# Kernel tuning notes

Measured on AMD Instinct MI355X. Metric: run time of the kernel, lower is better.

## Reference

```python
import jax, jax.numpy as jnp
import numpy as np
from math import ceil

N = 20000   # nodes
E = 320000  # edges
D = 128     # num_features == num_hidden
K = ceil(N * 0.1)  # 2000 PMA seeds


def _gcn(x, W, b, src, dst):
    # PyG GCNConv: add self-loops, symmetric deg^-1/2 normalization, sum-aggregate, bias
    n = x.shape[0]
    sl = jnp.arange(n)
    s = jnp.concatenate([src, sl])
    d = jnp.concatenate([dst, sl])
    deg = jax.ops.segment_sum(jnp.ones((s.shape[0],), x.dtype), d, num_segments=n)
    dinv = jax.lax.rsqrt(jnp.maximum(deg, 1e-12))
    norm = dinv[s] * dinv[d]
    h = x @ W
    return jax.ops.segment_sum(h[s] * norm[:, None], d, num_segments=n) + b


def _ln(x, g, b):
    m = jnp.mean(x, -1, keepdims=True)
    v = jnp.var(x, -1, keepdims=True)
    return (x - m) * jax.lax.rsqrt(v + 1e-5) * g + b


def setup_inputs() -> dict:
    key = jax.random.key(0)
    ks = jax.random.split(key, 32)
    w = lambda i, shape: jax.random.normal(ks[i], shape, jnp.float32) * 0.05
    z = lambda shape: jnp.zeros(shape, jnp.float32)
    o = lambda shape: jnp.ones(shape, jnp.float32)
    return {
        "x": jax.random.normal(ks[0], (N, D), jnp.float32),
        "edge_index": jax.random.randint(ks[1], (2, E), 0, N),
        "batch": jnp.zeros((N,), jnp.int32),
        "W1": w(2, (D, D)), "b1": z((D,)),
        "W2": w(3, (D, D)), "b2": z((D,)),
        "S": w(4, (1, K, D)),
        "Wq": w(5, (D, D)), "bq": z((D,)),
        "Wk": w(6, (D, D)), "bk": z((D,)),
        "Wv": w(7, (D, D)), "bv": z((D,)),
        "Wo": w(8, (D, D)), "bo": z((D,)),
        "g0": o((D,)), "be0": z((D,)),
        "g1": o((D,)), "be1": z((D,)),
        "Wl": w(9, (D, D)), "bl": z((D,)),
        "W3": w(10, (D, D)), "b3": z((D,)),
        "W4": w(11, (D, D)), "b4": z((D,)),
        "W5": w(12, (D, D)), "b5": z((D,)),
    }


def reference(x, edge_index, batch, W1, b1, W2, b2, S, Wq, bq, Wk, bk, Wv, bv,
              Wo, bo, g0, be0, g1, be1, Wl, bl, W3, b3, W4, b4, W5, b5):
    src, dst = edge_index[0], edge_index[1]
    h = jax.nn.relu(_gcn(x, W1, b1, src, dst))
    h = jax.nn.relu(_gcn(h, W2, b2, src, dst))
    # B=1 dense batch: mask all-true -> additive attention mask is 0
    Q = S @ Wq + bq                        # [1,K,D]
    Kd = _gcn(h, Wk, bk, src, dst)[None]   # [1,N,D]  (mab_conv='GCN')
    Vd = _gcn(h, Wv, bv, src, dst)[None]   # [1,N,D]
    score = jnp.einsum('bkd,bnd->bkn', Q, Kd) / jnp.sqrt(jnp.float32(D))
    A = jax.nn.softmax(score, axis=1)      # cluster=True: softmax over seed dim
    out = Q + jnp.einsum('bkn,bnd->bkd', A, Vd)
    out = _ln(out, g0, be0)
    out = out + jax.nn.relu(out @ Wo + bo)
    out = _ln(out, g1, be1)
    xl = out @ Wl + bl                     # [1,K,D]
    x_out = jnp.einsum('bkn,bkd->bnd', A, xl)[0]  # attn^T @ x -> [N,D], mask all-true
    h = jax.nn.relu(_gcn(x_out, W3, b3, src, dst))
    h = jax.nn.relu(_gcn(h, W4, b4, src, dst))
    return _gcn(h, W5, b5, src, dst)       # [N,D]
```

## Files before the change

kernel.cpp:

```cpp
#include <hip/hip_runtime.h>

#define NN 20000
#define EE 320000
#define KK 2000
#define KP 2048
#define SCALE 0.08838834764831845f
#define ZSPLIT 16
#define ACHUNKS 625
#define ZCH 4

typedef const float* cfp;
typedef __attribute__((ext_vector_type(8))) short sh8;
typedef __attribute__((ext_vector_type(4))) float f32x4;

static __device__ __forceinline__ float4 ld4(const float* p){ return *reinterpret_cast<const float4*>(p); }
static __device__ __forceinline__ void st4(float* p, float4 v){ *reinterpret_cast<float4*>(p) = v; }

static __device__ __forceinline__ unsigned short f2bf(float f){
    unsigned int u = __float_as_uint(f);
    u = (u + 0x7FFFu + ((u >> 16) & 1u)) >> 16;
    return (unsigned short)u;
}
static __device__ __forceinline__ float bf2f(unsigned short h){
    return __uint_as_float(((unsigned int)h) << 16);
}
static __device__ __forceinline__ sh8 lds8(const unsigned short* p){ return *reinterpret_cast<const sh8*>(p); }

static __device__ __forceinline__ void stage16(const unsigned short* g, unsigned short* l){
    __builtin_amdgcn_global_load_lds(
        (const __attribute__((address_space(1))) unsigned int*)g,
        (__attribute__((address_space(3))) unsigned int*)l, 16, 0, 0);
}

__global__ __launch_bounds__(256) void k_count(const int* dst, int* deg){
    int i = blockIdx.x*256 + threadIdx.x;
    if (i < EE) atomicAdd(&deg[dst[i]], 1);
}

__global__ __launch_bounds__(256) void k_dinv(const int* deg, float* dinv){
    int n = blockIdx.x*256 + threadIdx.x;
    if (n < NN) dinv[n] = rsqrtf((float)deg[n] + 1.0f);
}

__global__ __launch_bounds__(1024) void k_scan(const int* cnt, int* rows){
    __shared__ int part[1024];
    int t = threadIdx.x;
    int base = t*20;
    int s = 0;
    for (int i = 0; i < 20; ++i){ int idx = base+i; if (idx < NN) s += cnt[idx]; }
    part[t] = s; __syncthreads();
    for (int off = 1; off < 1024; off <<= 1){
        int v = (t >= off) ? part[t-off] : 0;
        __syncthreads();
        part[t] += v;
        __syncthreads();
    }
    int run = part[t] - s;
    for (int i = 0; i < 20; ++i){
        int idx = base+i;
        if (idx < NN){ rows[idx] = run; run += cnt[idx]; }
    }
    if (t == 0) rows[NN] = EE;
}

__global__ __launch_bounds__(256) void k_fill(const int* src, const int* dst, const int* rows,
                                              int* cursor, int* col){
    int i = blockIdx.x*256 + threadIdx.x;
    if (i < EE){
        int d = dst[i];
        int pos = rows[d] + atomicAdd(&cursor[d], 1);
        col[pos] = src[i];
    }
}

__global__ __launch_bounds__(256) void conv_wT(cfp w0, cfp w1, cfp w2, cfp w3, cfp w4, cfp w5, cfp w6,
                                               unsigned short* wts){
    const float* in;
    switch (blockIdx.z){
        case 0: in = w0; break; case 1: in = w1; break; case 2: in = w2; break;
        case 3: in = w3; break; case 4: in = w4; break; case 5: in = w5; break;
        default: in = w6; break;
    }
    unsigned short* out = wts + (size_t)blockIdx.z*16384;
    __shared__ float t[64][65];
    int r0 = blockIdx.x*64, c0 = blockIdx.y*64;
    int tid = threadIdx.x;
    for (int i = tid; i < 64*16; i += 256){
        int r = i >> 4, c4 = (i & 15) * 4;
        float4 v = ld4(in + (size_t)(r0+r)*128 + c0 + c4);
        t[r][c4+0]=v.x; t[r][c4+1]=v.y; t[r][c4+2]=v.z; t[r][c4+3]=v.w;
    }
    __syncthreads();
    for (int i = tid; i < 64*16; i += 256){
        int c = i >> 4, r4 = (i & 15) * 4;
        ushort4 o;
        o.x = f2bf(t[r4+0][c]); o.y = f2bf(t[r4+1][c]);
        o.z = f2bf(t[r4+2][c]); o.w = f2bf(t[r4+3][c]);
        *reinterpret_cast<ushort4*>(out + (size_t)(c0+c)*128 + r0 + r4) = o;
    }
}

__global__ __launch_bounds__(512) void gemm128(const float* __restrict__ A, const float* __restrict__ Wm,
                                               float* __restrict__ C, int M,
                                               const float* bias, const float* resid, int relu){
    __shared__ __align__(16) float Ws[128*132];
    __shared__ float As[64*129];
    int tid = threadIdx.x;
    int r0 = blockIdx.x*64;
    for (int i = tid; i < 128*32; i += 512){
        int r = i >> 5, c4 = (i & 31) * 4;
        float4 v = ld4(Wm + r*128 + c4);
        st4(&Ws[r*132 + c4], v);
    }
    for (int i = tid; i < 64*32; i += 512){
        int r = i >> 5, c4 = (i & 31) * 4;
// ... 96 lines not shown
    if (wid >= NN) return;
    int f = lane*2;
    ushort2 u = *reinterpret_cast<const ushort2*>(y + (size_t)wid*128 + f);
    float ax = bf2f(u.x), ay = bf2f(u.y);
    int s = rows[wid], e = rows[wid+1];
    int j = s;
    int e8 = s + ((e - s) & ~7);
    for (; j < e8; j += 8){
        ushort2 v[8];
        #pragma unroll
        for (int q = 0; q < 8; ++q){
            int c = col[j+q];
            v[q] = *reinterpret_cast<const ushort2*>(y + (size_t)c*128 + f);
        }
        #pragma unroll
        for (int q = 0; q < 8; ++q){ ax += bf2f(v[q].x); ay += bf2f(v[q].y); }
    }
    for (; j < e; ++j){
        int c0 = col[j];
        ushort2 v0 = *reinterpret_cast<const ushort2*>(y + (size_t)c0*128 + f);
        ax += bf2f(v0.x); ay += bf2f(v0.y);
    }
    float dn = dinv[wid];
    float ox = ax*dn + bias[f];
    float oy = ay*dn + bias[f+1];
    if (relu){ ox = fmaxf(ox, 0.f); oy = fmaxf(oy, 0.f); }
    if (out_fp32){
        *reinterpret_cast<float2*>((float*)outv + (size_t)wid*128 + f) = make_float2(ox, oy);
    } else {
        ushort2 o; o.x = f2bf(ox); o.y = f2bf(oy);
        *reinterpret_cast<ushort2*>((unsigned short*)outv + (size_t)wid*128 + f) = o;
    }
}

__global__ __launch_bounds__(256) void conv_bf16(const float* __restrict__ in, unsigned short* __restrict__ out, int n4){
    int i = blockIdx.x*256 + threadIdx.x;
    if (i < n4){
        float4 v = ld4(in + (size_t)i*4);
        ushort4 o;
        o.x = f2bf(v.x); o.y = f2bf(v.y); o.z = f2bf(v.z); o.w = f2bf(v.w);
        *reinterpret_cast<ushort4*>(out + (size_t)i*4) = o;
    }
}

__global__ __launch_bounds__(256) void conv_bf16_T(const float* __restrict__ in, unsigned short* __restrict__ out,
                                                   int M, int ldout, const float* __restrict__ rscale){
    __shared__ float t[64][65];
    int r0 = blockIdx.x*64, c0 = blockIdx.y*64;
    int tid = threadIdx.x;
    for (int i = tid; i < 64*16; i += 256){
        int r = i >> 4, c4 = (i & 15) * 4;
        float4 v = (r0 + r < M) ? ld4(in + (size_t)(r0+r)*128 + c0 + c4) : make_float4(0,0,0,0);
        if (rscale && r0 + r < M){
            float sc = rscale[r0 + r];
            v.x *= sc; v.y *= sc; v.z *= sc; v.w *= sc;
        }
        t[r][c4+0]=v.x; t[r][c4+1]=v.y; t[r][c4+2]=v.z; t[r][c4+3]=v.w;
    }
    __syncthreads();
    for (int i = tid; i < 64*16; i += 256){
        int c = i >> 4, r4 = (i & 15) * 4;
        if (r0 + r4 < M){
            ushort4 o;
            o.x = f2bf(t[r4+0][c]); o.y = f2bf(t[r4+1][c]);
            o.z = f2bf(t[r4+2][c]); o.w = f2bf(t[r4+3][c]);
            *reinterpret_cast<ushort4*>(out + (size_t)(c0+c)*ldout + r0 + r4) = o;
        }
    }
}

__global__ __launch_bounds__(256) void k_rcp32(const float* __restrict__ zp, const float* __restrict__ dinv,
                                               float* __restrict__ zinv, float* __restrict__ zdinv){
    int n = blockIdx.x*256 + threadIdx.x;
    if (n < NN){
        float s = 0.f;
        #pragma unroll
        for (int y = 0; y < ZCH; ++y) s += zp[(size_t)y*NN + n];
        float zi = 1.f / s;
        zinv[n] = zi;
        zdinv[n] = zi * dinv[n];
    }
}

__global__ __launch_bounds__(256) void s_gemm_exp(const unsigned short* __restrict__ Kb,
                                                  const unsigned short* __restrict__ Qb2,
                                                  unsigned short* __restrict__ E, float* __restrict__ zpart){
    __shared__ unsigned short Es[4][32*36];
    __shared__ float zsh[2][64];
    int tid = threadIdx.x;
    int wave = tid >> 6, lane = tid & 63;
    int wm = wave >> 1, wn = wave & 1;
    int n_blk = blockIdx.x*64;
    int k_base = blockIdx.y*512;
    int l15 = lane & 15;
    int h = lane >> 4;
    int roff = h * 8;
    int rq = h * 4;
    unsigned short* myEs = Es[wave];
    const unsigned short* ap0 = Kb + (size_t)(n_blk + wm*32 + l15)*128 + roff;
    const unsigned short* ap1 = ap0 + 16*128;
    sh8 a0[4], a1[4];
    #pragma unroll
    for (int r = 0; r < 4; ++r){ a0[r] = lds8(ap0 + r*32); a1[r] = lds8(ap1 + r*32); }
    const unsigned short* qbase = Qb2 + (size_t)(k_base + wn*32 + l15)*128 + roff;
    sh8 q0[4], q1[4];
    #pragma unroll
    for (int r = 0; r < 4; ++r){ q0[r] = lds8(qbase + r*32); q1[r] = lds8(qbase + 16*128 + r*32); }
    float zacc[2][4] = {{0.f,0.f,0.f,0.f},{0.f,0.f,0.f,0.f}};
    for (int kb = 0; kb < 8; ++kb){
        sh8 n0[4], n1[4];
        if (kb < 7){
            const unsigned short* qn = qbase + (size_t)(kb+1)*64*128;
            #pragma unroll
            for (int r = 0; r < 4; ++r){ n0[r] = lds8(qn + r*32); n1[r] = lds8(qn + 16*128 + r*32); }
        } else {
            #pragma unroll
            for (int r = 0; r < 4; ++r){ n0[r] = (sh8)0; n1[r] = (sh8)0; }
        }
        f32x4 acc00 = (f32x4)0.f, acc01 = (f32x4)0.f, acc10 = (f32x4)0.f, acc11 = (f32x4)0.f;
        #pragma unroll
        for (int r = 0; r < 4; ++r){
            acc00 = __builtin_amdgcn_mfma_f32_16x16x32_bf16(a0[r], q0[r], acc00, 0, 0, 0);
            acc01 = __builtin_amdgcn_mfma_f32_16x16x32_bf16(a0[r], q1[r], acc01, 0, 0, 0);
            acc10 = __builtin_amdgcn_mfma_f32_16x16x32_bf16(a1[r], q0[r], acc10, 0, 0, 0);
            acc11 = __builtin_amdgcn_mfma_f32_16x16x32_bf16(a1[r], q1[r], acc11, 0, 0, 0);
        }
        int kcol = k_base + kb*64;
        f32x4 accs[2][2] = {{acc00, acc01},{acc10, acc11}};
        #pragma unroll
        for (int mi = 0; mi < 2; ++mi){
            #pragma unroll
            for (int ni = 0; ni < 2; ++ni){
                f32x4 a = accs[mi][ni];
                bool kv = (kcol + wn*32 + ni*16 + l15) < KK;
                #pragma unroll
                for (int reg = 0; reg < 4; ++reg){
                    float e = kv ? __expf(a[reg]*SCALE) : 0.f;
                    myEs[(mi*16 + rq + reg)*36 + ni*16 + l15] = f2bf(e);
                    zacc[mi][reg] += e;
                }
            }
        }
        #pragma unroll
        for (int it = 0; it < 2; ++it){
            int r = it*16 + (lane >> 2);
            int q4 = (lane & 3) * 8;
            sh8 v = lds8(myEs + r*36 + q4);
            int gr = n_blk + wm*32 + r;
            if (gr < NN)
                *reinterpret_cast<sh8*>(E + (size_t)gr*KP + kcol + wn*32 + q4) = v;
        }
        #pragma unroll
        for (int r = 0; r < 4; ++r){ q0[r] = n0[r]; q1[r] = n1[r]; }
    }
    #pragma unroll
    for (int mi = 0; mi < 2; ++mi){
        #pragma unroll
        for (int reg = 0; reg < 4; ++reg){
            float v = zacc[mi][reg];
            v += __shfl_xor(v, 1);
            v += __shfl_xor(v, 2);
            v += __shfl_xor(v, 4);
            v += __shfl_xor(v, 8);
            zacc[mi][reg] = v;
        }
    }
    if (l15 == 0){
        #pragma unroll
        for (int mi = 0; mi < 2; ++mi)
            #pragma unroll
            for (int reg = 0; reg < 4; ++reg)
                zsh[wn][wm*32 + mi*16 + h*4 + reg] = zacc[mi][reg];
    }
    __syncthreads();
    if (tid < 64){
        int n = n_blk + tid;
        if (n < NN) zpart[(size_t)blockIdx.y*NN + n] = zsh[0][tid] + zsh[1][tid];
    }
}

__global__ __launch_bounds__(256) void attn_gemm(const unsigned short* __restrict__ E,
                                                 const unsigned short* __restrict__ Vt,
                                                 float* __restrict__ part){
    __shared__ unsigned short As[64*36];
    int tid = threadIdx.x;
    int wave = tid >> 6, lane = tid & 63;
    int kk0 = blockIdx.x*64;
    int per = (ACHUNKS + ZSPLIT - 1) / ZSPLIT;
    int c0 = blockIdx.y*per;
    int c1 = min(ACHUNKS, c0 + per);
    int l15 = lane & 15;
    int q8 = (lane >> 4) * 8;
    int d0 = wave*32;
    int n_l = tid & 31;
    int k8 = (tid >> 5) * 8;
    f32x4 acc[4][2];
    #pragma unroll
    for (int g = 0; g < 4; ++g){ acc[g][0] = (f32x4)0.f; acc[g][1] = (f32x4)0.f; }
    const unsigned short* ebase = E + (size_t)n_l*KP + kk0 + k8;
    const unsigned short* vb0p = Vt + (size_t)(d0 + l15)*NN + q8;
    const unsigned short* vb1p = vb0p + (size_t)16*NN;
    sh8 etmp = lds8(ebase + (size_t)c0*32*KP);
    sh8 vb0 = lds8(vb0p + c0*32);
    sh8 vb1 = lds8(vb1p + c0*32);
    for (int ch = c0; ch < c1; ++ch){
        unsigned short tmp[8];
        *reinterpret_cast<sh8*>(tmp) = etmp;
        #pragma unroll
        for (int j = 0; j < 8; ++j) As[(k8 + j)*36 + n_l] = tmp[j];
        __syncthreads();
        sh8 etn = (sh8)0, vbn0 = (sh8)0, vbn1 = (sh8)0;
        if (ch + 1 < c1){
            etn  = lds8(ebase + (size_t)(ch+1)*32*KP);
            vbn0 = lds8(vb0p + (ch+1)*32);
            vbn1 = lds8(vb1p + (ch+1)*32);
        }
        #pragma unroll
        for (int g = 0; g < 4; ++g){
            const unsigned short* ap = &As[(g*16 + l15)*36 + q8];
            union { struct { ushort4 lo, hi; } u; sh8 v; } af;
            af.u.lo = *reinterpret_cast<const ushort4*>(ap);
            af.u.hi = *reinterpret_cast<const ushort4*>(ap + 4);
            acc[g][0] = __builtin_amdgcn_mfma_f32_16x16x32_bf16(af.v, vb0, acc[g][0], 0, 0, 0);
            acc[g][1] = __builtin_amdgcn_mfma_f32_16x16x32_bf16(af.v, vb1, acc[g][1], 0, 0, 0);
        }
        __syncthreads();
        etmp = etn; vb0 = vbn0; vb1 = vbn1;
    }
    float* pbase = part + (size_t)blockIdx.y*KK*128;
    int rq = (lane >> 4) * 4;
    #pragma unroll
    for (int g = 0; g < 4; ++g){
        #pragma unroll
        for (int ni = 0; ni < 2; ++ni){
            int d = d0 + ni*16 + l15;
            #pragma unroll
            for (int reg = 0; reg < 4; ++reg){
                int kk = kk0 + g*16 + rq + reg;
                if (kk < KK) pbase[(size_t)kk*128 + d] = acc[g][ni][reg];
            }
        }
    }
}

__global__ __launch_bounds__(256) void xout_gemm(const unsigned short* __restrict__ E,
                                                 const unsigned short* __restrict__ B,
                                                 const float* __restrict__ zdinv,
                                                 unsigned short* __restrict__ out){
    __shared__ __align__(16) unsigned short ebuf[2][4096];
    int tid = threadIdx.x;
    int wave = tid >> 6, lane = tid & 63;
    int l15 = lane & 15;
    int h = lane >> 4;
    int m_base = blockIdx.x*32;
    int srow0 = wave*4 + h;
    int skb0  = (l15*16) ^ ((srow0 & 15) << 4);
    int srow1 = 16 + srow0;
    int skb1  = (l15*16) ^ ((srow1 & 15) << 4);
    const unsigned short* g0 = E + (size_t)(m_base + srow0)*KP + (skb0 >> 1);
    const unsigned short* g1 = E + (size_t)(m_base + srow1)*KP + (skb1 >> 1);
    unsigned short* l0 = &ebuf[0][wave*512];
    unsigned short* l1 = &ebuf[1][wave*512];
    const unsigned short* bp0 = B + (size_t)(wave*32 + l15)*KP + h*8;
    const unsigned short* bp1 = bp0 + (size_t)16*KP;
    int rswz = l15 << 4;

    f32x4 acc[2][2];
    #pragma unroll
    for (int mi = 0; mi < 2; ++mi)
        #pragma unroll
        for (int ni = 0; ni < 2; ++ni) acc[mi][ni] = (f32x4)0.f;

    stage16(g0, l0);
    stage16(g1, l0 + 2048);
    sh8 b0[4], b1[4];
    #pragma unroll
    for (int s = 0; s < 4; ++s){ b0[s] = lds8(bp0 + s*32); b1[s] = lds8(bp1 + s*32); }
    __syncthreads();

    for (int t = 0; t < 16; ++t){
        if (t < 15){
            const unsigned short* ng0 = g0 + (t+1)*128;
            const unsigned short* ng1 = g1 + (t+1)*128;
            unsigned short* nl = (t & 1) ? l0 : l1;
            stage16(ng0, nl);
            stage16(ng1, nl + 2048);
        }
        sh8 nb0[4], nb1[4];
        if (t < 15){
            #pragma unroll
            for (int s = 0; s < 4; ++s){
                nb0[s] = lds8(bp0 + (t+1)*128 + s*32);
                nb1[s] = lds8(bp1 + (t+1)*128 + s*32);
            }
        } else {
            #pragma unroll
            for (int s = 0; s < 4; ++s){ nb0[s] = (sh8)0; nb1[s] = (sh8)0; }
        }
        const unsigned short* eb = (t & 1) ? ebuf[1] : ebuf[0];
        #pragma unroll
        for (int s = 0; s < 4; ++s){
            int ko = ((h*16 + s*64) ^ rswz) >> 1;
            sh8 a0 = lds8(eb + l15*128 + ko);
            sh8 a1 = lds8(eb + (16 + l15)*128 + ko);
            acc[0][0] = __builtin_amdgcn_mfma_f32_16x16x32_bf16(a0, b0[s], acc[0][0], 0, 0, 0);
            acc[0][1] = __builtin_amdgcn_mfma_f32_16x16x32_bf16(a0, b1[s], acc[0][1], 0, 0, 0);
            acc[1][0] = __builtin_amdgcn_mfma_f32_16x16x32_bf16(a1, b0[s], acc[1][0], 0, 0, 0);
            acc[1][1] = __builtin_amdgcn_mfma_f32_16x16x32_bf16(a1, b1[s], acc[1][1], 0, 0, 0);
        }
        __syncthreads();
        #pragma unroll
        for (int s = 0; s < 4; ++s){ b0[s] = nb0[s]; b1[s] = nb1[s]; }
    }

    int rq = h*4;
    #pragma unroll
    for (int mi = 0; mi < 2; ++mi){
        #pragma unroll
        for (int ni = 0; ni < 2; ++ni){
            f32x4 a = acc[mi][ni];
            int d = wave*32 + ni*16 + l15;
            #pragma unroll
            for (int reg = 0; reg < 4; ++reg){
                int gm = m_base + mi*16 + rq + reg;
                out[(size_t)gm*128 + d] = f2bf(a[reg] * zdinv[gm]);
            }
        }
    }
}

__global__ __launch_bounds__(128) void ln_ker(const float* __restrict__ in, int nparts,
                                              const float* __restrict__ resid,
                                              const float* __restrict__ g, const float* __restrict__ be,
                                              float* __restrict__ out){
    __shared__ float rs[128], rq[128];
    int r = blockIdx.x, t = threadIdx.x;
    float v = 0.f;
    for (int p = 0; p < nparts; ++p) v += in[(size_t)p*KK*128 + r*128 + t];
    if (resid) v += resid[r*128 + t];
    rs[t] = v; rq[t] = v*v;
    __syncthreads();
    for (int off = 64; off > 0; off >>= 1){
        if (t < off){ rs[t] += rs[t+off]; rq[t] += rq[t+off]; }
        __syncthreads();
    }
    float mean = rs[0]*(1.f/128.f);
    float var = rq[0]*(1.f/128.f) - mean*mean;
    out[r*128 + t] = (v - mean)*rsqrtf(var + 1e-5f)*g[t] + be[t];
}

extern "C" void kernel_launch(void* const* d_in, const int* in_sizes, int n_in,
                              void* d_out, int out_size, void* d_ws, size_t ws_size,
                              hipStream_t stream){
    cfp x  = (cfp)d_in[0];
    const int* ei = (const int*)d_in[1];
    const int* esrc = ei;
    const int* edst = ei + EE;
    cfp W1=(cfp)d_in[3], b1=(cfp)d_in[4], W2=(cfp)d_in[5], b2=(cfp)d_in[6];
    cfp S =(cfp)d_in[7];
    cfp Wq=(cfp)d_in[8],  bq=(cfp)d_in[9],  Wk=(cfp)d_in[10], bk=(cfp)d_in[11];
    cfp Wv=(cfp)d_in[12], bv=(cfp)d_in[13], Wo=(cfp)d_in[14], bo=(cfp)d_in[15];
    cfp g0=(cfp)d_in[16], be0=(cfp)d_in[17], g1=(cfp)d_in[18], be1=(cfp)d_in[19];
    cfp Wl=(cfp)d_in[20], bl=(cfp)d_in[21], W3=(cfp)d_in[22], b3=(cfp)d_in[23];
    cfp W4=(cfp)d_in[24], b4=(cfp)d_in[25], W5=(cfp)d_in[26], b5=(cfp)d_in[27];

    char* wsb = (char*)d_ws;
    const size_t MB = 1048576;
    int*   deg    = (int*)  (wsb + 0);
    float* dinv   = (float*)(wsb + 81920);
    int*   rows   = (int*)  (wsb + 163840);
    int*   cursor = (int*)  (wsb + 245760);
    int*   col    = (int*)  (wsb + 327680);
    float* Qb     = (float*)(wsb + 2*MB);
    float* o1     = (float*)(wsb + 3*MB);
    float* o2     = (float*)(wsb + 4*MB);
    float* o3     = (float*)(wsb + 5*MB);
    float* xlb    = (float*)(wsb + 6*MB);
    float* zpart  = (float*)(wsb + 7*MB);
    float* zinv   = (float*)(wsb + 10*MB);
    float* zdinv  = (float*)(wsb + 10*MB + 131072);
    unsigned short* Wts  = (unsigned short*)(wsb + 10*MB + 262144);
    unsigned short* Qbf  = (unsigned short*)(wsb + 11*MB);
    unsigned short* xlt3 = (unsigned short*)(wsb + 11*MB + 524288);
    unsigned short* xbf = (unsigned short*)(wsb + 12*MB);
    unsigned short* h1  = (unsigned short*)(wsb + 17*MB);
    unsigned short* h2  = (unsigned short*)(wsb + 22*MB);
    unsigned short* ybuf= (unsigned short*)(wsb + 27*MB);
    unsigned short* Kbf = (unsigned short*)(wsb + 32*MB);
    unsigned short* Vtz = (unsigned short*)(wsb + 37*MB);
    float* NB3    = (float*)(wsb + 42*MB);
    float* part   = (float*)(wsb + 42*MB);
    unsigned short* E = (unsigned short*)(wsb + 62*MB);
    float* outp   = (float*)d_out;
    unsigned short* h3 = xbf;
    unsigned short* h4 = h1;

    (void)hipMemsetAsync(deg, 0, NN*sizeof(int), stream);
    (void)hipMemsetAsync(cursor, 0, NN*sizeof(int), stream);
    (void)hipMemsetAsync(xlt3, 0, 128*KP*sizeof(unsigned short), stream);

    k_count<<<1250, 256, 0, stream>>>(edst, deg);
    k_dinv<<<79, 256, 0, stream>>>(deg, dinv);
    k_scan<<<1, 1024, 0, stream>>>(deg, rows);
    k_fill<<<1250, 256, 0, stream>>>(esrc, edst, rows, cursor, col);

    conv_wT<<<dim3(2,2,7), 256, 0, stream>>>(W1, W2, Wk, Wv, W3, W4, W5, Wts);
    conv_bf16<<<2500, 256, 0, stream>>>(x, xbf, NN*32);
    unsigned short* W1t = Wts;
    unsigned short* W2t = Wts + 16384;
    unsigned short* Wkt = Wts + 2*16384;
    unsigned short* Wvt = Wts + 3*16384;
    unsigned short* W4t = Wts + 5*16384;
    unsigned short* W5t = Wts + 6*16384;

    const int GN = 313;
    const int GK = 32;

    tgemm<<<dim3(GN,2), 256, 0, stream>>>(xbf, NN, W1t, dinv, ybuf);
    gcn_agg_bf<<<5000, 256, 0, stream>>>(ybuf, dinv, rows, col, b1, h1, 1, 0);
    tgemm<<<dim3(GN,2), 256, 0, stream>>>(h1, NN, W2t, dinv, ybuf);
    gcn_agg_bf<<<5000, 256, 0, stream>>>(ybuf, dinv, rows, col, b2, h2, 1, 0);
    tgemm<<<dim3(GN,2), 256, 0, stream>>>(h2, NN, Wkt, dinv, ybuf);
    gcn_agg_bf<<<5000, 256, 0, stream>>>(ybuf, dinv, rows, col, bk, Kbf, 0, 0);
    gemm128<<<GK, 512, 0, stream>>>(S, Wq, Qb, KK, bq, nullptr, 0);
    conv_bf16<<<250, 256, 0, stream>>>(Qb, Qbf, KK*32);
    s_gemm_exp<<<dim3(GN, ZCH), 256, 0, stream>>>(Kbf, Qbf, E, zpart);
    k_rcp32<<<79, 256, 0, stream>>>(zpart, dinv, zinv, zdinv);
    tgemm<<<dim3(GN,2), 256, 0, stream>>>(h2, NN, Wvt, dinv, ybuf);
    gcn_agg_bf<<<5000, 256, 0, stream>>>(ybuf, dinv, rows, col, bv, NB3, 0, 1);
    conv_bf16_T<<<dim3(GN, 2), 256, 0, stream>>>(NB3, Vtz, NN, NN, zinv);
    attn_gemm<<<dim3(GK, ZSPLIT), 256, 0, stream>>>(E, Vtz, part);
    ln_ker<<<KK, 128, 0, stream>>>(part, ZSPLIT, Qb, g0, be0, o1);
    gemm128<<<GK, 512, 0, stream>>>(o1, Wo, o2, KK, bo, o1, 1);
    ln_ker<<<KK, 128, 0, stream>>>(o2, 1, nullptr, g1, be1, o3);
    gemm128<<<GK, 512, 0, stream>>>(o3, Wl, xlb, KK, bl, nullptr, 0);
    gemm128<<<GK, 512, 0, stream>>>(xlb, W3, o1, KK, nullptr, nullptr, 0);
    conv_bf16_T<<<dim3(GK, 2), 256, 0, stream>>>(o1, xlt3, KK, KP, nullptr);
    xout_gemm<<<625, 256, 0, stream>>>(E, xlt3, zdinv, ybuf);
    gcn_agg_bf<<<5000, 256, 0, stream>>>(ybuf, dinv, rows, col, b3, h3, 1, 0);
    tgemm<<<dim3(GN,2), 256, 0, stream>>>(h3, NN, W4t, dinv, ybuf);
    gcn_agg_bf<<<5000, 256, 0, stream>>>(ybuf, dinv, rows, col, b4, h4, 1, 0);
    tgemm<<<dim3(GN,2), 256, 0, stream>>>(h4, NN, W5t, dinv, ybuf);
    gcn_agg_bf<<<5000, 256, 0, stream>>>(ybuf, dinv, rows, col, b5, outp, 0, 1);
}
```

Before: 577.9 us.

## Swap MFMA operands in score kernel to store exp tiles directly without LDS

The score GEMM now puts Q as the A operand and K as the B operand, so each lane's accumulator registers hold four consecutive seed columns for one node. Those four bf16 exp values are written straight to global memory as a ushort4, which removes the shared-memory staging tile and its transpose round trip. The z row-sum reduction becomes a cross-half shuffle. The k range per block is halved (ZCH 4 to 8) to add more blocks, at the cost of more partial sums to add in the reciprocal kernel and narrower 8-byte global stores.

```diff
diff --git a/kernel.cpp b/kernel.cpp
--- a/kernel.cpp
+++ b/kernel.cpp
@@ -7,7 +7,7 @@
 #define SCALE 0.08838834764831845f
 #define ZSPLIT 16
 #define ACHUNKS 625
-#define ZCH 4
+#define ZCH 8
 
 typedef const float* cfp;
 typedef __attribute__((ext_vector_type(8))) short sh8;
@@ -296,31 +296,29 @@
 __global__ __launch_bounds__(256) void s_gemm_exp(const unsigned short* __restrict__ Kb,
                                                   const unsigned short* __restrict__ Qb2,
                                                   unsigned short* __restrict__ E, float* __restrict__ zpart){
-    __shared__ unsigned short Es[4][32*36];
     __shared__ float zsh[2][64];
     int tid = threadIdx.x;
     int wave = tid >> 6, lane = tid & 63;
     int wm = wave >> 1, wn = wave & 1;
     int n_blk = blockIdx.x*64;
-    int k_base = blockIdx.y*512;
+    int k_base = blockIdx.y*256;
     int l15 = lane & 15;
     int h = lane >> 4;
     int roff = h * 8;
     int rq = h * 4;
-    unsigned short* myEs = Es[wave];
-    const unsigned short* ap0 = Kb + (size_t)(n_blk + wm*32 + l15)*128 + roff;
-    const unsigned short* ap1 = ap0 + 16*128;
-    sh8 a0[4], a1[4];
-    #pragma unroll
-    for (int r = 0; r < 4; ++r){ a0[r] = lds8(ap0 + r*32); a1[r] = lds8(ap1 + r*32); }
+    const unsigned short* bp0 = Kb + (size_t)(n_blk + wm*32 + l15)*128 + roff;
+    const unsigned short* bp1 = bp0 + 16*128;
+    sh8 kd0[4], kd1[4];
+    #pragma unroll
+    for (int r = 0; r < 4; ++r){ kd0[r] = lds8(bp0 + r*32); kd1[r] = lds8(bp1 + r*32); }
     const unsigned short* qbase = Qb2 + (size_t)(k_base + wn*32 + l15)*128 + roff;
     sh8 q0[4], q1[4];
     #pragma unroll
     for (int r = 0; r < 4; ++r){ q0[r] = lds8(qbase + r*32); q1[r] = lds8(qbase + 16*128 + r*32); }
-    float zacc[2][4] = {{0.f,0.f,0.f,0.f},{0.f,0.f,0.f,0.f}};
-    for (int kb = 0; kb < 8; ++kb){
+    float zacc[2] = {0.f, 0.f};
+    for (int kb = 0; kb < 4; ++kb){
         sh8 n0[4], n1[4];
-        if (kb < 7){
+        if (kb < 3){
             const unsigned short* qn = qbase + (size_t)(kb+1)*64*128;
             #pragma unroll
             for (int r = 0; r < 4; ++r){ n0[r] = lds8(qn + r*32); n1[r] = lds8(qn + 16*128 + r*32); }
@@ -331,57 +329,44 @@
         f32x4 acc00 = (f32x4)0.f, acc01 = (f32x4)0.f, acc10 = (f32x4)0.f, acc11 = (f32x4)0.f;
         #pragma unroll
         for (int r = 0; r < 4; ++r){
-            acc00 = __builtin_amdgcn_mfma_f32_16x16x32_bf16(a0[r], q0[r], acc00, 0, 0, 0);
-            acc01 = __builtin_amdgcn_mfma_f32_16x16x32_bf16(a0[r], q1[r], acc01, 0, 0, 0);
-            acc10 = __builtin_amdgcn_mfma_f32_16x16x32_bf16(a1[r], q0[r], acc10, 0, 0, 0);
-            acc11 = __builtin_amdgcn_mfma_f32_16x16x32_bf16(a1[r], q1[r], acc11, 0, 0, 0);
-        }
-        int kcol = k_base + kb*64;
+            acc00 = __builtin_amdgcn_mfma_f32_16x16x32_bf16(q0[r], kd0[r], acc00, 0, 0, 0);
+            acc01 = __builtin_amdgcn_mfma_f32_16x16x32_bf16(q0[r], kd1[r], acc01, 0, 0, 0);
+            acc10 = __builtin_amdgcn_mfma_f32_16x16x32_bf16(q1[r], kd0[r], acc10, 0, 0, 0);
+            acc11 = __builtin_amdgcn_mfma_f32_16x16x32_bf16(q1[r], kd1[r], acc11, 0, 0, 0);
+        }
+        int kcol = k_base + kb*64 + wn*32;
         f32x4 accs[2][2] = {{acc00, acc01},{acc10, acc11}};
         #pragma unroll
-        for (int mi = 0; mi < 2; ++mi){
+        for (int ki = 0; ki < 2; ++ki){
             #pragma unroll
             for (int ni = 0; ni < 2; ++ni){
-                f32x4 a = accs[mi][ni];
-                bool kv = (kcol + wn*32 + ni*16 + l15) < KK;
-                #pragma unroll
-                for (int reg = 0; reg < 4; ++reg){
-                    float e = kv ? __expf(a[reg]*SCALE) : 0.f;
-                    myEs[(mi*16 + rq + reg)*36 + ni*16 + l15] = f2bf(e);
-                    zacc[mi][reg] += e;
-                }
-            }
-        }
-        #pragma unroll
-        for (int it = 0; it < 2; ++it){
-            int r = it*16 + (lane >> 2);
-            int q4 = (lane & 3) * 8;
-            sh8 v = lds8(myEs + r*36 + q4);
-            int gr = n_blk + wm*32 + r;
-            if (gr < NN)
-                *reinterpret_cast<sh8*>(E + (size_t)gr*KP + kcol + wn*32 + q4) = v;
+                f32x4 a = accs[ki][ni];
+                int k0 = kcol + ki*16 + rq;
+                int n  = n_blk + wm*32 + ni*16 + l15;
+                ushort4 o;
+                float e0 = (k0 + 0 < KK) ? __expf(a[0]*SCALE) : 0.f;
+                float e1 = (k0 + 1 < KK) ? __expf(a[1]*SCALE) : 0.f;
+                float e2 = (k0 + 2 < KK) ? __expf(a[2]*SCALE) : 0.f;
+                float e3 = (k0 + 3 < KK) ? __expf(a[3]*SCALE) : 0.f;
+                o.x = f2bf(e0); o.y = f2bf(e1); o.z = f2bf(e2); o.w = f2bf(e3);
+                zacc[ni] += (e0 + e1) + (e2 + e3);
+                if (n < NN)
+                    *reinterpret_cast<ushort4*>(E + (size_t)n*KP + k0) = o;
+            }
         }
         #pragma unroll
         for (int r = 0; r < 4; ++r){ q0[r] = n0[r]; q1[r] = n1[r]; }
     }
     #pragma unroll
-    for (int mi = 0; mi < 2; ++mi){
-        #pragma unroll
-        for (int reg = 0; reg < 4; ++reg){
-            float v = zacc[mi][reg];
-            v += __shfl_xor(v, 1);
-            v += __shfl_xor(v, 2);
-            v += __shfl_xor(v, 4);
-            v += __shfl_xor(v, 8);
-            zacc[mi][reg] = v;
-        }
-    }
-    if (l15 == 0){
-        #pragma unroll
-        for (int mi = 0; mi < 2; ++mi)
-            #pragma unroll
-            for (int reg = 0; reg < 4; ++reg)
-                zsh[wn][wm*32 + mi*16 + h*4 + reg] = zacc[mi][reg];
+    for (int ni = 0; ni < 2; ++ni){
+        float v = zacc[ni];
+        v += __shfl_xor(v, 16);
+        v += __shfl_xor(v, 32);
+        zacc[ni] = v;
+    }
+    if (h == 0){
+        zsh[wn][wm*32 + l15]      = zacc[0];
+        zsh[wn][wm*32 + 16 + l15] = zacc[1];
     }
     __syncthreads();
     if (tid < 64){
```

After: 584.4 us. No clear change (+1.1%).

## Recompute attention exponentials on the fly instead of materialising E matrix

Applied to the files above, without the earlier changes.

Stops writing the N×KP bf16 exponential matrix E to global memory; the score pass now only produces softmax denominators. The attention·V and A^T·xl GEMMs each recompute K·Q scores with MFMA, apply exp in registers, stage the result through LDS and consume it immediately. This removes roughly 80MB of E traffic (one write and two reads) at the cost of doing the QK^T GEMM and exp three times. The split count changes to cover 64-row node chunks, and Vt is zeroed beforehand so padded tail reads are safe.

```diff
diff --git a/kernel.cpp b/kernel.cpp
--- a/kernel.cpp
+++ b/kernel.cpp
@@ -5,8 +5,8 @@
 #define KK 2000
 #define KP 2048
 #define SCALE 0.08838834764831845f
-#define ZSPLIT 16
-#define ACHUNKS 625
+#define ZSPLIT 20
+#define NCH 313
 #define ZCH 4
 
 typedef const float* cfp;
@@ -25,12 +25,6 @@
     return __uint_as_float(((unsigned int)h) << 16);
 }
 static __device__ __forceinline__ sh8 lds8(const unsigned short* p){ return *reinterpret_cast<const sh8*>(p); }
-
-static __device__ __forceinline__ void stage16(const unsigned short* g, unsigned short* l){
-    __builtin_amdgcn_global_load_lds(
-        (const __attribute__((address_space(1))) unsigned int*)g,
-        (__attribute__((address_space(3))) unsigned int*)l, 16, 0, 0);
-}
 
 __global__ __launch_bounds__(256) void k_count(const int* dst, int* deg){
     int i = blockIdx.x*256 + threadIdx.x;
@@ -293,10 +287,9 @@
     }
 }
 
-__global__ __launch_bounds__(256) void s_gemm_exp(const unsigned short* __restrict__ Kb,
-                                                  const unsigned short* __restrict__ Qb2,
-                                                  unsigned short* __restrict__ E, float* __restrict__ zpart){
-    __shared__ unsigned short Es[4][32*36];
+__global__ __launch_bounds__(256) void z_pass(const unsigned short* __restrict__ Kb,
+                                              const unsigned short* __restrict__ Qb2,
+                                              float* __restrict__ zpart){
     __shared__ float zsh[2][64];
     int tid = threadIdx.x;
     int wave = tid >> 6, lane = tid & 63;
@@ -306,8 +299,6 @@
     int l15 = lane & 15;
     int h = lane >> 4;
     int roff = h * 8;
-    int rq = h * 4;
-    unsigned short* myEs = Es[wave];
     const unsigned short* ap0 = Kb + (size_t)(n_blk + wm*32 + l15)*128 + roff;
     const unsigned short* ap1 = ap0 + 16*128;
     sh8 a0[4], a1[4];
@@ -347,19 +338,9 @@
                 #pragma unroll
                 for (int reg = 0; reg < 4; ++reg){
                     float e = kv ? __expf(a[reg]*SCALE) : 0.f;
-                    myEs[(mi*16 + rq + reg)*36 + ni*16 + l15] = f2bf(e);
                     zacc[mi][reg] += e;
                 }
             }
-        }
-        #pragma unroll
-        for (int it = 0; it < 2; ++it){
-            int r = it*16 + (lane >> 2);
-            int q4 = (lane & 3) * 8;
-            sh8 v = lds8(myEs + r*36 + q4);
-            int gr = n_blk + wm*32 + r;
-            if (gr < NN)
-                *reinterpret_cast<sh8*>(E + (size_t)gr*KP + kcol + wn*32 + q4) = v;
         }
         #pragma unroll
         for (int r = 0; r < 4; ++r){ q0[r] = n0[r]; q1[r] = n1[r]; }
@@ -390,151 +371,163 @@
     }
 }
 
-__global__ __launch_bounds__(256) void attn_gemm(const unsigned short* __restrict__ E,
-                                                 const unsigned short* __restrict__ Vt,
-                                                 float* __restrict__ part){
-    __shared__ unsigned short As[64*36];
+__global__ __launch_bounds__(256) void attn_fused(const unsigned short* __restrict__ Kb,
+                                                  const unsigned short* __restrict__ Qb2,
+                                                  const unsigned short* __restrict__ Vt,
+                                                  float* __restrict__ part){
+    __shared__ __align__(16) unsigned short Et[64*72];
     int tid = threadIdx.x;
     int wave = tid >> 6, lane = tid & 63;
-    int kk0 = blockIdx.x*64;
-    int per = (ACHUNKS + ZSPLIT - 1) / ZSPLIT;
+    int wm = wave >> 1, wn = wave & 1;
+    int l15 = lane & 15;
+    int h = lane >> 4;
+    int roff = h*8, rq = h*4;
+    int kblk = blockIdx.x*64;
+    int per = (NCH + ZSPLIT - 1) / ZSPLIT;
     int c0 = blockIdx.y*per;
-    int c1 = min(ACHUNKS, c0 + per);
-    int l15 = lane & 15;
-    int q8 = (lane >> 4) * 8;
+    int c1 = min(NCH, c0 + per);
+    const unsigned short* qp0 = Qb2 + (size_t)(kblk + wn*32 + l15)*128 + roff;
+    const unsigned short* qp1 = qp0 + 16*128;
+    sh8 q0[4], q1[4];
+    #pragma unroll
+    for (int r = 0; r < 4; ++r){ q0[r] = lds8(qp0 + r*32); q1[r] = lds8(qp1 + r*32); }
     int d0 = wave*32;
-    int n_l = tid & 31;
-    int k8 = (tid >> 5) * 8;
+    const unsigned short* vrow0 = Vt + (size_t)(d0 + l15)*NN;
+    const unsigned short* vrow1 = Vt + (size_t)(d0 + 16 + l15)*NN;
     f32x4 acc[4][2];
     #pragma unroll
-    for (int g = 0; g < 4; ++g){ acc[g][0] = (f32x4)0.f; acc[g][1] = (f32x4)0.f; }
-    const unsigned short* ebase = E + (size_t)n_l*KP + kk0 + k8;
-    const unsigned short* vb0p = Vt + (size_t)(d0 + l15)*NN + q8;
-    const unsigned short* vb1p = vb0p + (size_t)16*NN;
-    sh8 etmp = lds8(ebase + (size_t)c0*32*KP);
-    sh8 vb0 = lds8(vb0p + c0*32);
-    sh8 vb1 = lds8(vb1p + c0*32);
+    for (int ks = 0; ks < 4; ++ks){ acc[ks][0] = (f32x4)0.f; acc[ks][1] = (f32x4)0.f; }
     for (int ch = c0; ch < c1; ++ch){
-        unsigned short tmp[8];
-        *reinterpret_cast<sh8*>(tmp) = etmp;
-        #pragma unroll
-        for (int j = 0; j < 8; ++j) As[(k8 + j)*36 + n_l] = tmp[j];
+        int nch = ch*64;
+        const unsigned short* kp0 = Kb + (size_t)(nch + wm*32 + l15)*128 + roff;
+        const unsigned short* kp1 = kp0 + 16*128;
+        f32x4 c00 = (f32x4)0.f, c01 = (f32x4)0.f, c10 = (f32x4)0.f, c11 = (f32x4)0.f;
+        #pragma unroll
+        for (int r = 0; r < 4; ++r){
+            sh8 a0 = lds8(kp0 + r*32);
+            sh8 a1 = lds8(kp1 + r*32);
+            c00 = __builtin_amdgcn_mfma_f32_16x16x32_bf16(a0, q0[r], c00, 0, 0, 0);
+            c01 = __builtin_amdgcn_mfma_f32_16x16x32_bf16(a0, q1[r], c01, 0, 0, 0);
+            c10 = __builtin_amdgcn_mfma_f32_16x16x32_bf16(a1, q0[r], c10, 0, 0, 0);
+            c11 = __builtin_amdgcn_mfma_f32_16x16x32_bf16(a1, q1[r], c11, 0, 0, 0);
+        }
         __syncthreads();
-        sh8 etn = (sh8)0, vbn0 = (sh8)0, vbn1 = (sh8)0;
-        if (ch + 1 < c1){
-            etn  = lds8(ebase + (size_t)(ch+1)*32*KP);
-            vbn0 = lds8(vb0p + (ch+1)*32);
-            vbn1 = lds8(vb1p + (ch+1)*32);
-        }
-        #pragma unroll
-        for (int g = 0; g < 4; ++g){
-            const unsigned short* ap = &As[(g*16 + l15)*36 + q8];
-            union { struct { ushort4 lo, hi; } u; sh8 v; } af;
-            af.u.lo = *reinterpret_cast<const ushort4*>(ap);
-            af.u.hi = *reinterpret_cast<const ushort4*>(ap + 4);
-            acc[g][0] = __builtin_amdgcn_mfma_f32_16x16x32_bf16(af.v, vb0, acc[g][0], 0, 0, 0);
-            acc[g][1] = __builtin_amdgcn_mfma_f32_16x16x32_bf16(af.v, vb1, acc[g][1], 0, 0, 0);
+        f32x4 cs[2][2] = {{c00, c01},{c10, c11}};
+        #pragma unroll
+        for (int mi = 0; mi < 2; ++mi){
+            #pragma unroll
+            for (int ni = 0; ni < 2; ++ni){
+                f32x4 a = cs[mi][ni];
+                int kloc = wn*32 + ni*16 + l15;
+                bool kvv = (kblk + kloc) < KK;
+                #pragma unroll
+                for (int reg = 0; reg < 4; ++reg){
+                    int n = nch + wm*32 + mi*16 + rq + reg;
+                    float e = (kvv && n < NN) ? __expf(a[reg]*SCALE) : 0.f;
+                    Et[kloc*72 + wm*32 + mi*16 + rq + reg] = f2bf(e);
+                }
+            }
         }
         __syncthreads();
-        etmp = etn; vb0 = vbn0; vb1 = vbn1;
+        #pragma unroll
+        for (int ns = 0; ns < 2; ++ns){
+            sh8 vb0 = lds8(vrow0 + nch + ns*32 + roff);
+            sh8 vb1 = lds8(vrow1 + nch + ns*32 + roff);
+            #pragma unroll
+            for (int ks = 0; ks < 4; ++ks){
+                sh8 af = lds8(Et + (ks*16 + l15)*72 + ns*32 + roff);
+                acc[ks][0] = __builtin_amdgcn_mfma_f32_16x16x32_bf16(af, vb0, acc[ks][0], 0, 0, 0);
+                acc[ks][1] = __builtin_amdgcn_mfma_f32_16x16x32_bf16(af, vb1, acc[ks][1], 0, 0, 0);
+            }
+        }
     }
     float* pbase = part + (size_t)blockIdx.y*KK*128;
-    int rq = (lane >> 4) * 4;
-    #pragma unroll
-    for (int g = 0; g < 4; ++g){
-        #pragma unroll
-        for (int ni = 0; ni < 2; ++ni){
-            int d = d0 + ni*16 + l15;
+    #pragma unroll
+    for (int ks = 0; ks < 4; ++ks){
+        #pragma unroll
+        for (int ds = 0; ds < 2; ++ds){
+            f32x4 a = acc[ks][ds];
+            int d = d0 + ds*16 + l15;
             #pragma unroll
             for (int reg = 0; reg < 4; ++reg){
-                int kk = kk0 + g*16 + rq + reg;
-                if (kk < KK) pbase[(size_t)kk*128 + d] = acc[g][ni][reg];
-            }
-        }
-    }
-}
-
-__global__ __launch_bounds__(256) void xout_gemm(const unsigned short* __restrict__ E,
-                                                 const unsigned short* __restrict__ B,
-                                                 const float* __restrict__ zdinv,
-                                                 unsigned short* __restrict__ out){
-    __shared__ __align__(16) unsigned short ebuf[2][4096];
+                int k = kblk + ks*16 + rq + reg;
+                if (k < KK) pbase[(size_t)k*128 + d] = a[reg];
+            }
+        }
+    }
+}
+
+__global__ __launch_bounds__(256) void xout_fused(const unsigned short* __restrict__ Kb,
+                                                  const unsigned short* __restrict__ Qb2,
+                                                  const unsigned short* __restrict__ Bx,
+                                                  const float* __restrict__ zdinv,
+                                                  unsigned short* __restrict__ out){
+    __shared__ __align__(16) unsigned short El[32*72];
     int tid = threadIdx.x;
     int wave = tid >> 6, lane = tid & 63;
+    int wm = wave >> 1, wn = wave & 1;
     int l15 = lane & 15;
     int h = lane >> 4;
-    int m_base = blockIdx.x*32;
-    int srow0 = wave*4 + h;
-    int skb0  = (l15*16) ^ ((srow0 & 15) << 4);
-    int srow1 = 16 + srow0;
-    int skb1  = (l15*16) ^ ((srow1 & 15) << 4);
-    const unsigned short* g0 = E + (size_t)(m_base + srow0)*KP + (skb0 >> 1);
-    const unsigned short* g1 = E + (size_t)(m_base + srow1)*KP + (skb1 >> 1);
-    unsigned short* l0 = &ebuf[0][wave*512];
-    unsigned short* l1 = &ebuf[1][wave*512];
-    const unsigned short* bp0 = B + (size_t)(wave*32 + l15)*KP + h*8;
-    const unsigned short* bp1 = bp0 + (size_t)16*KP;
-    int rswz = l15 << 4;
-
+    int roff = h*8, rq = h*4;
+    int n_blk = blockIdx.x*32;
+    const unsigned short* kp = Kb + (size_t)(n_blk + wm*16 + l15)*128 + roff;
+    sh8 kd[4];
+    #pragma unroll
+    for (int r = 0; r < 4; ++r) kd[r] = lds8(kp + r*32);
+    int d0 = wave*32;
+    const unsigned short* bx0 = Bx + (size_t)(d0 + l15)*KP;
+    const unsigned short* bx1 = Bx + (size_t)(d0 + 16 + l15)*KP;
     f32x4 acc[2][2];
     #pragma unroll
-    for (int mi = 0; mi < 2; ++mi)
-        #pragma unroll
-        for (int ni = 0; ni < 2; ++ni) acc[mi][ni] = (f32x4)0.f;
-
-    stage16(g0, l0);
-    stage16(g1, l0 + 2048);
-    sh8 b0[4], b1[4];
-    #pragma unroll
-    for (int s = 0; s < 4; ++s){ b0[s] = lds8(bp0 + s*32); b1[s] = lds8(bp1 + s*32); }
-    __syncthreads();
-
-    for (int t = 0; t < 16; ++t){
-        if (t < 15){
-            const unsigned short* ng0 = g0 + (t+1)*128;
-            const unsigned short* ng1 = g1 + (t+1)*128;
-            unsigned short* nl = (t & 1) ? l0 : l1;
-            stage16(ng0, nl);
-            stage16(ng1, nl + 2048);
-        }
-        sh8 nb0[4], nb1[4];
-        if (t < 15){
-            #pragma unroll
-            for (int s = 0; s < 4; ++s){
-                nb0[s] = lds8(bp0 + (t+1)*128 + s*32);
-                nb1[s] = lds8(bp1 + (t+1)*128 + s*32);
-            }
-        } else {
-            #pragma unroll
-            for (int s = 0; s < 4; ++s){ nb0[s] = (sh8)0; nb1[s] = (sh8)0; }
-        }
-        const unsigned short* eb = (t & 1) ? ebuf[1] : ebuf[0];
-        #pragma unroll
-        for (int s = 0; s < 4; ++s){
-            int ko = ((h*16 + s*64) ^ rswz) >> 1;
-            sh8 a0 = lds8(eb + l15*128 + ko);
-            sh8 a1 = lds8(eb + (16 + l15)*128 + ko);
-            acc[0][0] = __builtin_amdgcn_mfma_f32_16x16x32_bf16(a0, b0[s], acc[0][0], 0, 0, 0);
-            acc[0][1] = __builtin_amdgcn_mfma_f32_16x16x32_bf16(a0, b1[s], acc[0][1], 0, 0, 0);
-            acc[1][0] = __builtin_amdgcn_mfma_f32_16x16x32_bf16(a1, b0[s], acc[1][0], 0, 0, 0);
-            acc[1][1] = __builtin_amdgcn_mfma_f32_16x16x32_bf16(a1, b1[s], acc[1][1], 0, 0, 0);
+    for (int ns = 0; ns < 2; ++ns){ acc[ns][0] = (f32x4)0.f; acc[ns][1] = (f32x4)0.f; }
+    for (int kc = 0; kc < 32; ++kc){
+        int kk0 = kc*64;
+        const unsigned short* qp0 = Qb2 + (size_t)(kk0 + wn*32 + l15)*128 + roff;
+        const unsigned short* qp1 = qp0 + 16*128;
+        f32x4 c0v = (f32x4)0.f, c1v = (f32x4)0.f;
+        #pragma unroll
+        for (int r = 0; r < 4; ++r){
+            sh8 qa = lds8(qp0 + r*32);
+            sh8 qb = lds8(qp1 + r*32);
+            c0v = __builtin_amdgcn_mfma_f32_16x16x32_bf16(kd[r], qa, c0v, 0, 0, 0);
+            c1v = __builtin_amdgcn_mfma_f32_16x16x32_bf16(kd[r], qb, c1v, 0, 0, 0);
         }
         __syncthreads();
         #pragma unroll
-        for (int s = 0; s < 4; ++s){ b0[s] = nb0[s]; b1[s] = nb1[s]; }
-    }
-
-    int rq = h*4;
-    #pragma unroll
-    for (int mi = 0; mi < 2; ++mi){
-        #pragma unroll
         for (int ni = 0; ni < 2; ++ni){
-            f32x4 a = acc[mi][ni];
-            int d = wave*32 + ni*16 + l15;
+            f32x4 a = ni ? c1v : c0v;
+            int kloc = wn*32 + ni*16 + l15;
+            bool kvv = (kk0 + kloc) < KK;
             #pragma unroll
             for (int reg = 0; reg < 4; ++reg){
-                int gm = m_base + mi*16 + rq + reg;
-                out[(size_t)gm*128 + d] = f2bf(a[reg] * zdinv[gm]);
+                int nloc = wm*16 + rq + reg;
+                float e = kvv ? __expf(a[reg]*SCALE) : 0.f;
+                El[nloc*72 + kloc] = f2bf(e);
+            }
+        }
+        __syncthreads();
+        #pragma unroll
+        for (int ks = 0; ks < 2; ++ks){
+            sh8 b0 = lds8(bx0 + kk0 + ks*32 + roff);
+            sh8 b1 = lds8(bx1 + kk0 + ks*32 + roff);
+            #pragma unroll
+            for (int ns = 0; ns < 2; ++ns){
+                sh8 af = lds8(El + (ns*16 + l15)*72 + ks*32 + roff);
+                acc[ns][0] = __builtin_amdgcn_mfma_f32_16x16x32_bf16(af, b0, acc[ns][0], 0, 0, 0);
+                acc[ns][1] = __builtin_amdgcn_mfma_f32_16x16x32_bf16(af, b1, acc[ns][1], 0, 0, 0);
+            }
+        }
+    }
+    #pragma unroll
+    for (int ns = 0; ns < 2; ++ns){
+        #pragma unroll
+        for (int ds = 0; ds < 2; ++ds){
+            f32x4 a = acc[ns][ds];
+            int d = d0 + ds*16 + l15;
+            #pragma unroll
+            for (int reg = 0; reg < 4; ++reg){
+                int n = n_blk + ns*16 + rq + reg;
+                out[(size_t)n*128 + d] = f2bf(a[reg] * zdinv[n]);
             }
         }
     }
@@ -601,7 +594,6 @@
     unsigned short* Vtz = (unsigned short*)(wsb + 37*MB);
     float* NB3    = (float*)(wsb + 42*MB);
     float* part   = (float*)(wsb + 42*MB);
-    unsigned short* E = (unsigned short*)(wsb + 62*MB);
     float* outp   = (float*)d_out;
     unsigned short* h3 = xbf;
     unsigned short* h4 = h1;
@@ -609,6 +601,7 @@
     (void)hipMemsetAsync(deg, 0, NN*sizeof(int), stream);
     (void)hipMemsetAsync(cursor, 0, NN*sizeof(int), stream);
     (void)hipMemsetAsync(xlt3, 0, 128*KP*sizeof(unsigned short), stream);
+    (void)hipMemsetAsync(Vtz, 0, 5*MB, stream);
 
     k_count<<<1250, 256, 0, stream>>>(edst, deg);
     k_dinv<<<79, 256, 0, stream>>>(deg, dinv);
@@ -635,19 +628,19 @@
     gcn_agg_bf<<<5000, 256, 0, stream>>>(ybuf, dinv, rows, col, bk, Kbf, 0, 0);
     gemm128<<<GK, 512, 0, stream>>>(S, Wq, Qb, KK, bq, nullptr, 0);
     conv_bf16<<<250, 256, 0, stream>>>(Qb, Qbf, KK*32);
-    s_gemm_exp<<<dim3(GN, ZCH), 256, 0, stream>>>(Kbf, Qbf, E, zpart);
+    z_pass<<<dim3(GN, ZCH), 256, 0, stream>>>(Kbf, Qbf, zpart);
     k_rcp32<<<79, 256, 0, stream>>>(zpart, dinv, zinv, zdinv);
     tgemm<<<dim3(GN,2), 256, 0, stream>>>(h2, NN, Wvt, dinv, ybuf);
     gcn_agg_bf<<<5000, 256, 0, stream>>>(ybuf, dinv, rows, col, bv, NB3, 0, 1);
     conv_bf16_T<<<dim3(GN, 2), 256, 0, stream>>>(NB3, Vtz, NN, NN, zinv);
-    attn_gemm<<<dim3(GK, ZSPLIT), 256, 0, stream>>>(E, Vtz, part);
+    attn_fused<<<dim3(GK, ZSPLIT), 256, 0, stream>>>(Kbf, Qbf, Vtz, part);
     ln_ker<<<KK, 128, 0, stream>>>(part, ZSPLIT, Qb, g0, be0, o1);
     gemm128<<<GK, 512, 0, stream>>>(o1, Wo, o2, KK, bo, o1, 1);
     ln_ker<<<KK, 128, 0, stream>>>(o2, 1, nullptr, g1, be1, o3);
     gemm128<<<GK, 512, 0, stream>>>(o3, Wl, xlb, KK, bl, nullptr, 0);
     gemm128<<<GK, 512, 0, stream>>>(xlb, W3, o1, KK, nullptr, nullptr, 0);
     conv_bf16_T<<<dim3(GK, 2), 256, 0, stream>>>(o1, xlt3, KK, KP, nullptr);
-    xout_gemm<<<625, 256, 0, stream>>>(E, xlt3, zdinv, ybuf);
+    xout_fused<<<625, 256, 0, stream>>>(Kbf, Qbf, xlt3, zdinv, ybuf);
     gcn_agg_bf<<<5000, 256, 0, stream>>>(ybuf, dinv, rows, col, b3, h3, 1, 0);
     tgemm<<<dim3(GN,2), 256, 0, stream>>>(h3, NN, W4t, dinv, ybuf);
     gcn_agg_bf<<<5000, 256, 0, stream>>>(ybuf, dinv, rows, col, b4, h4, 1, 0);
```

After: 685.5 us. 1.19x slower.

## Store exp-score matrix in 512-column chunk-major layout with full-row block writeback

Applied to the files above, without the earlier changes.

The bf16 exp-score matrix E changes from row-major [N][2048] to four chunk-major slabs [4][N][512]. s_gemm_exp buffers the whole 64x512 tile in shared memory and writes contiguous 1KB rows once at the end, instead of scattered 64-byte stores per k-block. attn_gemm and xout_gemm index the new layout. The aim is more contiguous global writes and reads of E, at the cost of about 65KB of LDS per block in s_gemm_exp, which may lower occupancy.

```diff
diff --git a/kernel.cpp b/kernel.cpp
--- a/kernel.cpp
+++ b/kernel.cpp
@@ -296,7 +296,7 @@
 __global__ __launch_bounds__(256) void s_gemm_exp(const unsigned short* __restrict__ Kb,
                                                   const unsigned short* __restrict__ Qb2,
                                                   unsigned short* __restrict__ E, float* __restrict__ zpart){
-    __shared__ unsigned short Es[4][32*36];
+    __shared__ __align__(16) unsigned short Eb[64*520];
     __shared__ float zsh[2][64];
     int tid = threadIdx.x;
     int wave = tid >> 6, lane = tid & 63;
@@ -307,7 +307,6 @@
     int h = lane >> 4;
     int roff = h * 8;
     int rq = h * 4;
-    unsigned short* myEs = Es[wave];
     const unsigned short* ap0 = Kb + (size_t)(n_blk + wm*32 + l15)*128 + roff;
     const unsigned short* ap1 = ap0 + 16*128;
     sh8 a0[4], a1[4];
@@ -336,30 +335,21 @@
             acc10 = __builtin_amdgcn_mfma_f32_16x16x32_bf16(a1[r], q0[r], acc10, 0, 0, 0);
             acc11 = __builtin_amdgcn_mfma_f32_16x16x32_bf16(a1[r], q1[r], acc11, 0, 0, 0);
         }
-        int kcol = k_base + kb*64;
+        int kcol = kb*64;
         f32x4 accs[2][2] = {{acc00, acc01},{acc10, acc11}};
         #pragma unroll
         for (int mi = 0; mi < 2; ++mi){
             #pragma unroll
             for (int ni = 0; ni < 2; ++ni){
                 f32x4 a = accs[mi][ni];
-                bool kv = (kcol + wn*32 + ni*16 + l15) < KK;
+                bool kv = (k_base + kcol + wn*32 + ni*16 + l15) < KK;
                 #pragma unroll
                 for (int reg = 0; reg < 4; ++reg){
                     float e = kv ? __expf(a[reg]*SCALE) : 0.f;
-                    myEs[(mi*16 + rq + reg)*36 + ni*16 + l15] = f2bf(e);
+                    Eb[(wm*32 + mi*16 + rq + reg)*520 + kcol + wn*32 + ni*16 + l15] = f2bf(e);
                     zacc[mi][reg] += e;
                 }
             }
-        }
-        #pragma unroll
-        for (int it = 0; it < 2; ++it){
-            int r = it*16 + (lane >> 2);
-            int q4 = (lane & 3) * 8;
-            sh8 v = lds8(myEs + r*36 + q4);
-            int gr = n_blk + wm*32 + r;
-            if (gr < NN)
-                *reinterpret_cast<sh8*>(E + (size_t)gr*KP + kcol + wn*32 + q4) = v;
         }
         #pragma unroll
         for (int r = 0; r < 4; ++r){ q0[r] = n0[r]; q1[r] = n1[r]; }
@@ -388,6 +378,14 @@
         int n = n_blk + tid;
         if (n < NN) zpart[(size_t)blockIdx.y*NN + n] = zsh[0][tid] + zsh[1][tid];
     }
+    unsigned short* ebase = E + ((size_t)blockIdx.y*NN + n_blk)*512;
+    #pragma unroll
+    for (int it = 0; it < 16; ++it){
+        int row = it*4 + wave;
+        sh8 v = lds8(Eb + row*520 + lane*8);
+        if (n_blk + row < NN)
+            *reinterpret_cast<sh8*>(ebase + (size_t)row*512 + lane*8) = v;
+    }
 }
 
 __global__ __launch_bounds__(256) void attn_gemm(const unsigned short* __restrict__ E,
@@ -397,6 +395,8 @@
     int tid = threadIdx.x;
     int wave = tid >> 6, lane = tid & 63;
     int kk0 = blockIdx.x*64;
+    int kch = kk0 >> 9;
+    int ko  = kk0 & 511;
     int per = (ACHUNKS + ZSPLIT - 1) / ZSPLIT;
     int c0 = blockIdx.y*per;
     int c1 = min(ACHUNKS, c0 + per);
@@ -408,10 +408,10 @@
     f32x4 acc[4][2];
     #pragma unroll
     for (int g = 0; g < 4; ++g){ acc[g][0] = (f32x4)0.f; acc[g][1] = (f32x4)0.f; }
-    const unsigned short* ebase = E + (size_t)n_l*KP + kk0 + k8;
+    const unsigned short* ebase = E + ((size_t)kch*NN + n_l)*512 + ko + k8;
     const unsigned short* vb0p = Vt + (size_t)(d0 + l15)*NN + q8;
     const unsigned short* vb1p = vb0p + (size_t)16*NN;
-    sh8 etmp = lds8(ebase + (size_t)c0*32*KP);
+    sh8 etmp = lds8(ebase + (size_t)c0*32*512);
     sh8 vb0 = lds8(vb0p + c0*32);
     sh8 vb1 = lds8(vb1p + c0*32);
     for (int ch = c0; ch < c1; ++ch){
@@ -422,7 +422,7 @@
         __syncthreads();
         sh8 etn = (sh8)0, vbn0 = (sh8)0, vbn1 = (sh8)0;
         if (ch + 1 < c1){
-            etn  = lds8(ebase + (size_t)(ch+1)*32*KP);
+            etn  = lds8(ebase + (size_t)(ch+1)*32*512);
             vbn0 = lds8(vb0p + (ch+1)*32);
             vbn1 = lds8(vb1p + (ch+1)*32);
         }
@@ -468,13 +468,12 @@
     int skb0  = (l15*16) ^ ((srow0 & 15) << 4);
     int srow1 = 16 + srow0;
     int skb1  = (l15*16) ^ ((srow1 & 15) << 4);
-    const unsigned short* g0 = E + (size_t)(m_base + srow0)*KP + (skb0 >> 1);
-    const unsigned short* g1 = E + (size_t)(m_base + srow1)*KP + (skb1 >> 1);
     unsigned short* l0 = &ebuf[0][wave*512];
     unsigned short* l1 = &ebuf[1][wave*512];
     const unsigned short* bp0 = B + (size_t)(wave*32 + l15)*KP + h*8;
     const unsigned short* bp1 = bp0 + (size_t)16*KP;
     int rswz = l15 << 4;
+    #define EADDR(t, srow, skb) (E + (((size_t)((t) >> 2))*NN + m_base + (srow))*512 + ((t) & 3)*128 + ((skb) >> 1))
 
     f32x4 acc[2][2];
     #pragma unroll
@@ -482,8 +481,8 @@
         #pragma unroll
         for (int ni = 0; ni < 2; ++ni) acc[mi][ni] = (f32x4)0.f;
 
-    stage16(g0, l0);
-    stage16(g1, l0 + 2048);
+    stage16(EADDR(0, srow0, skb0), l0);
+    stage16(EADDR(0, srow1, skb1), l0 + 2048);
     sh8 b0[4], b1[4];
     #pragma unroll
     for (int s = 0; s < 4; ++s){ b0[s] = lds8(bp0 + s*32); b1[s] = lds8(bp1 + s*32); }
@@ -491,11 +490,9 @@
 
     for (int t = 0; t < 16; ++t){
         if (t < 15){
-            const unsigned short* ng0 = g0 + (t+1)*128;
-            const unsigned short* ng1 = g1 + (t+1)*128;
             unsigned short* nl = (t & 1) ? l0 : l1;
-            stage16(ng0, nl);
-            stage16(ng1, nl + 2048);
+            stage16(EADDR(t+1, srow0, skb0), nl);
+            stage16(EADDR(t+1, srow1, skb1), nl + 2048);
         }
         sh8 nb0[4], nb1[4];
         if (t < 15){
@@ -523,6 +520,7 @@
         #pragma unroll
         for (int s = 0; s < 4; ++s){ b0[s] = nb0[s]; b1[s] = nb1[s]; }
     }
+    #undef EADDR
 
     int rq = h*4;
     #pragma unroll
```

Result: no change. 586.4 us (+1.5%).
